# Kernel optimization log

Hardware: AMD Instinct MI355X
Metric: run time of the kernel (lower is better)

## Reference

```python
import jax, jax.numpy as jnp
import numpy as np

N = 50000   # nodes
E = 800000  # edges (avg degree 16)
IN, H, OUT = 128, 128, 128


def _lin(key, fan_in, fan_out):
    s = 1.0 / np.sqrt(fan_in)
    return jax.random.uniform(key, (fan_in, fan_out), minval=-s, maxval=s, dtype=jnp.float32)


def setup_inputs() -> dict:
    key = jax.random.key(0)
    ks = jax.random.split(key, 12)
    inp = {
        "x": jax.random.normal(ks[0], (N, IN), dtype=jnp.float32),
        "edge_index": jax.random.randint(ks[1], (2, E), 0, N, dtype=jnp.int64),
        # layer 1: in -> hidden
        "Wl1": _lin(ks[2], IN, H), "b1": jnp.zeros((H,), jnp.float32), "Wr1": _lin(ks[3], IN, H),
        # layer 2: hidden -> hidden
        "Wl2": _lin(ks[4], H, H), "b2": jnp.zeros((H,), jnp.float32), "Wr2": _lin(ks[5], H, H),
        # layer 3: hidden -> out
        "Wl3": _lin(ks[6], H, OUT), "b3": jnp.zeros((OUT,), jnp.float32), "Wr3": _lin(ks[7], H, OUT),
    }
    return inp


def _sage_conv(x, src, dst, inv_deg, Wl, b, Wr):
    # mean-aggregate neighbor messages: gather from src, scatter-sum to dst
    msg = jnp.take(x, src, axis=0)                       # [E, d]
    agg = jax.ops.segment_sum(msg, dst, num_segments=N)  # [N, d]
    mean = agg * inv_deg[:, None]                        # scatter-mean (0 for isolated)
    return mean @ Wl + b + x @ Wr


def reference(x, edge_index, Wl1, b1, Wr1, Wl2, b2, Wr2, Wl3, b3, Wr3):
    src, dst = edge_index[0], edge_index[1]
    deg = jax.ops.segment_sum(jnp.ones((E,), jnp.float32), dst, num_segments=N)
    inv_deg = jnp.where(deg > 0, 1.0 / jnp.maximum(deg, 1.0), 0.0)

    h = _sage_conv(x, src, dst, inv_deg, Wl1, b1, Wr1)
    h = jax.nn.relu(h)  # dropout p=0.5 is identity in eval mode
    h = _sage_conv(h, src, dst, inv_deg, Wl2, b2, Wr2)
    h = jax.nn.relu(h)
    h = _sage_conv(h, src, dst, inv_deg, Wl3, b3, Wr3)
    return h
```

## Files before the change

kernel.cpp:

```cpp
#include <hip/hip_runtime.h>


#define D 128

typedef __attribute__((ext_vector_type(8))) short bf16x8;
typedef __attribute__((ext_vector_type(4))) float f32x4;

__device__ inline ushort f2bf(float f) {
  union { float f; unsigned u; } v; v.f = f;
  unsigned r = v.u + 0x7fffu + ((v.u >> 16) & 1u);
  return (ushort)(r >> 16);
}
__device__ inline float bf2f(ushort h) {
  union { unsigned u; float f; } v; v.u = ((unsigned)h) << 16;
  return v.f;
}

__global__ __launch_bounds__(256) void k_bhist(const int* __restrict__ dst,
                                               int* __restrict__ bhist, int E, int NB) {
  __shared__ int h[512];
  int t = threadIdx.x;
  for (int i = t; i < NB; i += 256) h[i] = 0;
  __syncthreads();
  int beg = blockIdx.x * 4096;
  int end = min(beg + 4096, E);
  for (int i = beg + t; i < end; i += 256) atomicAdd(&h[dst[i] >> 7], 1);
  __syncthreads();
  for (int i = t; i < NB; i += 256)
    if (h[i]) atomicAdd(&bhist[i], h[i]);
}

__global__ __launch_bounds__(512) void k_bscan(const int* __restrict__ bhist,
                                               int* __restrict__ bbase,
                                               int* __restrict__ bcur,
                                               int* __restrict__ offN, int NB) {
  __shared__ int part[512];
  int t = threadIdx.x;
  part[t] = (t < NB) ? bhist[t] : 0;
  __syncthreads();
  for (int d = 1; d < 512; d <<= 1) {
    int x = part[t];
    int a = (t >= d) ? part[t - d] : 0;
    __syncthreads();
    part[t] = x + a;
    __syncthreads();
  }
  if (t < NB) {
    int b = (t == 0) ? 0 : part[t - 1];
    bbase[t] = b;
    bcur[t] = b;
  }
  if (t == NB - 1) *offN = part[t];
}

__global__ __launch_bounds__(256) void k_bucket(const int* __restrict__ src,
                                                const int* __restrict__ dst,
                                                int* __restrict__ bcur,
                                                unsigned* __restrict__ ebuf,
                                                int E, int NB) {
  __shared__ int h[512];
  __shared__ int base[512];
  int t = threadIdx.x;
  for (int i = t; i < NB; i += 256) h[i] = 0;
  __syncthreads();
  int beg = blockIdx.x * 4096;
  int end = min(beg + 4096, E);
  for (int i = beg + t; i < end; i += 256) atomicAdd(&h[dst[i] >> 7], 1);
  __syncthreads();
  for (int i = t; i < NB; i += 256) {
    int c = h[i];
    base[i] = c ? atomicAdd(&bcur[i], c) : 0;
    h[i] = 0;
  }
  __syncthreads();
  for (int i = beg + t; i < end; i += 256) {
    int d = dst[i];
    int b = d >> 7;
    int r = atomicAdd(&h[b], 1);
    ebuf[base[b] + r] = (((unsigned)src[i]) << 16) | (unsigned)d;
  }
}

__global__ __launch_bounds__(256) void k_csr(const unsigned* __restrict__ ebuf,
                                             const int* __restrict__ bbase,
                                             const int* __restrict__ bhist,
                                             int* __restrict__ off,
                                             float* __restrict__ invd,
                                             int* __restrict__ srcs, int N) {
  __shared__ int dcount[128];
  __shared__ int dloc[128];
  int b = blockIdx.x;
  int t = threadIdx.x;
  int beg = bbase[b];
  int end = beg + bhist[b];
  if (t < 128) dcount[t] = 0;
  __syncthreads();
  for (int i = beg + t; i < end; i += 256) atomicAdd(&dcount[ebuf[i] & 127], 1);
  __syncthreads();
  if (t < 128) dloc[t] = dcount[t];
  __syncthreads();
  for (int d = 1; d < 128; d <<= 1) {
    int x = 0, a = 0;
    if (t < 128) {
      x = dloc[t];
      if (t >= d) a = dloc[t - d];
    }
    __syncthreads();
    if (t < 128) dloc[t] = x + a;
    __syncthreads();
  }
  if (t < 128) {
    int node = b * 128 + t;
    if (node < N) {
      int ex = beg + dloc[t] - dcount[t];
      off[node] = ex;
      int c = dcount[t];
      invd[node] = c > 0 ? 1.0f / (float)c : 0.0f;
      dcount[t] = ex;
    }
  }
  __syncthreads();
  for (int i = beg + t; i < end; i += 256) {
    unsigned p = ebuf[i];
    int slot = atomicAdd(&dcount[p & 127], 1);
    srcs[slot] = (int)(p >> 16);
  }
}

__global__ void k_cast(const float* __restrict__ x, ushort* __restrict__ xb, int total4) {
  int i = blockIdx.x * blockDim.x + threadIdx.x;
  if (i >= total4) return;
  float4 v = *reinterpret_cast<const float4*>(x + (size_t)i * 4);
  ushort4 o;
  o.x = f2bf(v.x); o.y = f2bf(v.y); o.z = f2bf(v.z); o.w = f2bf(v.w);
  *reinterpret_cast<ushort4*>(xb + (size_t)i * 4) = o;
}

__global__ void k_pack3(const float* __restrict__ Wl1, const float* __restrict__ Wr1,
                        const float* __restrict__ Wl2, const float* __restrict__ Wr2,
                        const float* __restrict__ Wl3, const float* __restrict__ Wr3,
                        ushort* __restrict__ Bp) {
  int gidx = blockIdx.x * blockDim.x + threadIdx.x;
  int layer = gidx >> 15;
  int idx = gidx & 32767;
  const float* Wl = (layer == 0) ? Wl1 : (layer == 1) ? Wl2 : Wl3;
  const float* Wr = (layer == 0) ? Wr1 : (layer == 1) ? Wr2 : Wr3;
  int kk = idx >> 12;
  int ct = (idx >> 9) & 7;
  int l  = (idx >> 3) & 63;
  int j  = idx & 7;
  int k = kk * 32 + ((l >> 4) << 3) + j;
  int col = ct * 16 + (l & 15);
  float v = (k < 128) ? Wl[k * 128 + col] : Wr[(k - 128) * 128 + col];
  Bp[gidx] = f2bf(v);
}

__global__ __launch_bounds__(256) void k_gather(const ushort* __restrict__ hin,
                                                const int* __restrict__ off,
                                                const int* __restrict__ srcs,
                                                const float* __restrict__ invd,
                                                ushort* __restrict__ meanb, int N) {
  int wid = blockIdx.x * 4 + (threadIdx.x >> 6);
  if (wid >= N) return;
  int lane = threadIdx.x & 63;
  int g = lane >> 4;
  int s = lane & 15;
  int lo = off[wid], hi = off[wid + 1];

  float acc[8] = {0.f, 0.f, 0.f, 0.f, 0.f, 0.f, 0.f, 0.f};
  int e = lo + g;
  for (; e + 4 < hi; e += 8) {
    int i0 = srcs[e];
    int i1 = srcs[e + 4];
    bf16x8 v0 = *reinterpret_cast<const bf16x8*>(hin + (size_t)i0 * D + s * 8);
    bf16x8 v1 = *reinterpret_cast<const bf16x8*>(hin + (size_t)i1 * D + s * 8);
#pragma unroll
    for (int j = 0; j < 8; ++j) acc[j] += bf2f((ushort)v0[j]);
#pragma unroll
    for (int j = 0; j < 8; ++j) acc[j] += bf2f((ushort)v1[j]);
  }
  if (e < hi) {
    int i0 = srcs[e];
    bf16x8 v0 = *reinterpret_cast<const bf16x8*>(hin + (size_t)i0 * D + s * 8);
#pragma unroll
    for (int j = 0; j < 8; ++j) acc[j] += bf2f((ushort)v0[j]);
  }

#pragma unroll
  for (int j = 0; j < 8; ++j) acc[j] += __shfl_xor(acc[j], 16);
#pragma unroll
  for (int j = 0; j < 8; ++j) acc[j] += __shfl_xor(acc[j], 32);

  if (lane < 16) {
    float w = invd[wid];
    bf16x8 o;
#pragma unroll
    for (int j = 0; j < 8; ++j) o[j] = (short)f2bf(acc[j] * w);
    *reinterpret_cast<bf16x8*>(meanb + (size_t)wid * D + s * 8) = o;
  }
}

template <int RELU, int FINAL>
__global__ __launch_bounds__(256) void k_combine(const ushort* __restrict__ meanb,
                                                 const ushort* __restrict__ hb,
                                                 const ushort* __restrict__ Bpack,
                                                 const float* __restrict__ bias,
                                                 float* __restrict__ outf,
                                                 ushort* __restrict__ outh, int N) {
  int l = threadIdx.x & 63;
  int w = threadIdx.x >> 6;
  int row0 = blockIdx.x * 64 + w * 16;
  int lr = l & 15;
  int kgrp = l >> 4;
  int arow = row0 + lr;
  if (arow >= N) arow = N - 1;
  size_t abase = (size_t)arow * D;

  f32x4 acc[8];
#pragma unroll
  for (int ct = 0; ct < 8; ++ct) {
    float bv = bias[ct * 16 + lr];
    acc[ct] = (f32x4){bv, bv, bv, bv};
  }

#pragma unroll
  for (int kk = 0; kk < 8; ++kk) {
    const ushort* asrc = (kk < 4) ? meanb : hb;
    int klocal = ((kk & 3) << 5) + (kgrp << 3);
    bf16x8 a = *reinterpret_cast<const bf16x8*>(asrc + abase + klocal);
    const ushort* bb = Bpack + ((size_t)kk << 12) + ((size_t)l << 3);
#pragma unroll
    for (int ct = 0; ct < 8; ++ct) {
      bf16x8 b = *reinterpret_cast<const bf16x8*>(bb + (ct << 9));
      acc[ct] = __builtin_amdgcn_mfma_f32_16x16x32_bf16(a, b, acc[ct], 0, 0, 0);
    }
  }

#pragma unroll
  for (int ct = 0; ct < 8; ++ct) {
    int c = ct * 16 + lr;
#pragma unroll
    for (int r = 0; r < 4; ++r) {
      int rr = row0 + kgrp * 4 + r;
      if (rr < N) {
        float v = acc[ct][r];
        if (RELU) v = fmaxf(v, 0.f);
        if (FINAL) outf[(size_t)rr * D + c] = v;
        else outh[(size_t)rr * D + c] = f2bf(v);
      }
    }
  }
}

extern "C" void kernel_launch(void* const* d_in, const int* in_sizes, int n_in,
                              void* d_out, int out_size, void* d_ws, size_t ws_size,
                              hipStream_t stream) {
  const float* x   = (const float*)d_in[0];
  const int*   ei  = (const int*)d_in[1];
  const float* Wl1 = (const float*)d_in[2];
  const float* b1  = (const float*)d_in[3];
  const float* Wr1 = (const float*)d_in[4];
  const float* Wl2 = (const float*)d_in[5];
  const float* b2  = (const float*)d_in[6];
  const float* Wr2 = (const float*)d_in[7];
  const float* Wl3 = (const float*)d_in[8];
  const float* b3  = (const float*)d_in[9];
  const float* Wr3 = (const float*)d_in[10];
  float* out = (float*)d_out;

  int N = in_sizes[0] / D;
  int E = in_sizes[1] / 2;
  const int* srcp = ei;
  const int* dstp = ei + E;
  int NB = (N + 127) >> 7;

  char* p = (char*)d_ws;
  auto carve = [&](size_t bytes) {
    void* r = (void*)p;
    p += (bytes + 255) & ~(size_t)255;
    return r;
  };
  int*      bhist = (int*)carve((size_t)512 * 4);
  int*      bbase = (int*)carve((size_t)512 * 4);
  int*      bcur  = (int*)carve((size_t)512 * 4);
  int*      off   = (int*)carve((size_t)(N + 1) * 4);
  float*    invd  = (float*)carve((size_t)N * 4);
  int*      srcs  = (int*)carve((size_t)E * 4);
  unsigned* ebuf  = (unsigned*)carve((size_t)E * 4);
  ushort*   xb    = (ushort*)carve((size_t)N * D * 2);
  ushort*   h1b   = (ushort*)carve((size_t)N * D * 2);
  ushort*   h2b   = (ushort*)carve((size_t)N * D * 2);
  ushort*   meanb = (ushort*)carve((size_t)N * D * 2);
  ushort*   Bp    = (ushort*)carve((size_t)3 * 32768 * 2);

  hipMemsetAsync(bhist, 0, (size_t)NB * 4, stream);
  int ch_blocks = (E + 4095) / 4096;
  k_bhist<<<ch_blocks, 256, 0, stream>>>(dstp, bhist, E, NB);
  k_bscan<<<1, 512, 0, stream>>>(bhist, bbase, bcur, off + N, NB);
  k_bucket<<<ch_blocks, 256, 0, stream>>>(srcp, dstp, bcur, ebuf, E, NB);
  k_csr<<<NB, 256, 0, stream>>>(ebuf, bbase, bhist, off, invd, srcs, N);

  int total4 = N * D / 4;
  k_cast<<<(total4 + 255) / 256, 256, 0, stream>>>(x, xb, total4);
  k_pack3<<<3 * 32768 / 256, 256, 0, stream>>>(Wl1, Wr1, Wl2, Wr2, Wl3, Wr3, Bp);

  int gather_blocks  = (N + 3) / 4;
  int combine_blocks = (N + 63) / 64;

  k_gather<<<gather_blocks, 256, 0, stream>>>(xb, off, srcs, invd, meanb, N);
  k_combine<1, 0><<<combine_blocks, 256, 0, stream>>>(meanb, xb, Bp, b1, nullptr, h1b, N);
  k_gather<<<gather_blocks, 256, 0, stream>>>(h1b, off, srcs, invd, meanb, N);
  k_combine<1, 0><<<combine_blocks, 256, 0, stream>>>(meanb, h1b, Bp + 32768, b2, nullptr, h2b, N);
  k_gather<<<gather_blocks, 256, 0, stream>>>(h2b, off, srcs, invd, meanb, N);
  k_combine<0, 1><<<combine_blocks, 256, 0, stream>>>(meanb, h2b, Bp + 2 * 32768, b3, out, nullptr, N);
}
```

Measured before the change: 197.6 us.

## Fuse neighbor gather and MFMA combine into one kernel per layer

Merges the per-layer gather (mean aggregation) and combine (dual GEMM) kernels into one kernel. Each block aggregates 16 nodes into a swizzled LDS tile, then the four waves split the 128 output columns, two 16-wide tiles each. This removes the meanb round trip through global memory and half the launches. In exchange each block now does a small 16-row GEMM, so weight-fragment loads are amortized over fewer rows, and the gather and MFMA phases within a block are serialized by a barrier.

```diff
diff --git a/kernel.cpp b/kernel.cpp
--- a/kernel.cpp
+++ b/kernel.cpp
@@ -155,95 +155,102 @@
   Bp[gidx] = f2bf(v);
 }
 
-__global__ __launch_bounds__(256) void k_gather(const ushort* __restrict__ hin,
-                                                const int* __restrict__ off,
-                                                const int* __restrict__ srcs,
-                                                const float* __restrict__ invd,
-                                                ushort* __restrict__ meanb, int N) {
-  int wid = blockIdx.x * 4 + (threadIdx.x >> 6);
-  if (wid >= N) return;
-  int lane = threadIdx.x & 63;
+template <int RELU, int FINAL>
+__global__ __launch_bounds__(256, 6) void k_fused(const ushort* __restrict__ hin,
+                                                  const int* __restrict__ off,
+                                                  const int* __restrict__ srcs,
+                                                  const float* __restrict__ invd,
+                                                  const ushort* __restrict__ Bpack,
+                                                  const float* __restrict__ bias,
+                                                  float* __restrict__ outf,
+                                                  ushort* __restrict__ outh, int N) {
+  __shared__ ushort smean[16 * D];
+  int t = threadIdx.x;
+  int w = t >> 6;
+  int lane = t & 63;
+  int node0 = blockIdx.x * 16;
   int g = lane >> 4;
   int s = lane & 15;
-  int lo = off[wid], hi = off[wid + 1];
-
-  float acc[8] = {0.f, 0.f, 0.f, 0.f, 0.f, 0.f, 0.f, 0.f};
-  int e = lo + g;
-  for (; e + 4 < hi; e += 8) {
-    int i0 = srcs[e];
-    int i1 = srcs[e + 4];
-    bf16x8 v0 = *reinterpret_cast<const bf16x8*>(hin + (size_t)i0 * D + s * 8);
-    bf16x8 v1 = *reinterpret_cast<const bf16x8*>(hin + (size_t)i1 * D + s * 8);
-#pragma unroll
-    for (int j = 0; j < 8; ++j) acc[j] += bf2f((ushort)v0[j]);
-#pragma unroll
-    for (int j = 0; j < 8; ++j) acc[j] += bf2f((ushort)v1[j]);
-  }
-  if (e < hi) {
-    int i0 = srcs[e];
-    bf16x8 v0 = *reinterpret_cast<const bf16x8*>(hin + (size_t)i0 * D + s * 8);
-#pragma unroll
-    for (int j = 0; j < 8; ++j) acc[j] += bf2f((ushort)v0[j]);
-  }
-
-#pragma unroll
-  for (int j = 0; j < 8; ++j) acc[j] += __shfl_xor(acc[j], 16);
-#pragma unroll
-  for (int j = 0; j < 8; ++j) acc[j] += __shfl_xor(acc[j], 32);
-
-  if (lane < 16) {
-    float w = invd[wid];
-    bf16x8 o;
-#pragma unroll
-    for (int j = 0; j < 8; ++j) o[j] = (short)f2bf(acc[j] * w);
-    *reinterpret_cast<bf16x8*>(meanb + (size_t)wid * D + s * 8) = o;
-  }
-}
-
-template <int RELU, int FINAL>
-__global__ __launch_bounds__(256) void k_combine(const ushort* __restrict__ meanb,
-                                                 const ushort* __restrict__ hb,
-                                                 const ushort* __restrict__ Bpack,
-                                                 const float* __restrict__ bias,
-                                                 float* __restrict__ outf,
-                                                 ushort* __restrict__ outh, int N) {
-  int l = threadIdx.x & 63;
-  int w = threadIdx.x >> 6;
-  int row0 = blockIdx.x * 64 + w * 16;
-  int lr = l & 15;
-  int kgrp = l >> 4;
-  int arow = row0 + lr;
+
+  for (int q = 0; q < 4; ++q) {
+    int nl = w * 4 + q;
+    int n = node0 + nl;
+    float acc[8] = {0.f, 0.f, 0.f, 0.f, 0.f, 0.f, 0.f, 0.f};
+    float wgt = 0.f;
+    if (n < N) {
+      wgt = invd[n];
+      int lo = off[n], hi = off[n + 1];
+      int e = lo + g;
+      for (; e + 4 < hi; e += 8) {
+        int i0 = srcs[e];
+        int i1 = srcs[e + 4];
+        bf16x8 v0 = *reinterpret_cast<const bf16x8*>(hin + (size_t)i0 * D + s * 8);
+        bf16x8 v1 = *reinterpret_cast<const bf16x8*>(hin + (size_t)i1 * D + s * 8);
+#pragma unroll
+        for (int j = 0; j < 8; ++j) acc[j] += bf2f((ushort)v0[j]);
+#pragma unroll
+        for (int j = 0; j < 8; ++j) acc[j] += bf2f((ushort)v1[j]);
+      }
+      if (e < hi) {
+        int i0 = srcs[e];
+        bf16x8 v0 = *reinterpret_cast<const bf16x8*>(hin + (size_t)i0 * D + s * 8);
+#pragma unroll
+        for (int j = 0; j < 8; ++j) acc[j] += bf2f((ushort)v0[j]);
+      }
+    }
+#pragma unroll
+    for (int j = 0; j < 8; ++j) acc[j] += __shfl_xor(acc[j], 16);
+#pragma unroll
+    for (int j = 0; j < 8; ++j) acc[j] += __shfl_xor(acc[j], 32);
+    if (lane < 16) {
+      bf16x8 o;
+#pragma unroll
+      for (int j = 0; j < 8; ++j) o[j] = (short)f2bf(acc[j] * wgt);
+      int byte = nl * 256 + ((s * 16) ^ ((nl & 7) << 4));
+      *reinterpret_cast<bf16x8*>(reinterpret_cast<char*>(smean) + byte) = o;
+    }
+  }
+  __syncthreads();
+
+  int lr = lane & 15;
+  int kgrp = lane >> 4;
+  int arow = node0 + lr;
   if (arow >= N) arow = N - 1;
   size_t abase = (size_t)arow * D;
 
-  f32x4 acc[8];
-#pragma unroll
-  for (int ct = 0; ct < 8; ++ct) {
-    float bv = bias[ct * 16 + lr];
-    acc[ct] = (f32x4){bv, bv, bv, bv};
+  f32x4 acc2[2];
+#pragma unroll
+  for (int i = 0; i < 2; ++i) {
+    float bv = bias[(w * 2 + i) * 16 + lr];
+    acc2[i] = (f32x4){bv, bv, bv, bv};
   }
 
 #pragma unroll
   for (int kk = 0; kk < 8; ++kk) {
-    const ushort* asrc = (kk < 4) ? meanb : hb;
     int klocal = ((kk & 3) << 5) + (kgrp << 3);
-    bf16x8 a = *reinterpret_cast<const bf16x8*>(asrc + abase + klocal);
-    const ushort* bb = Bpack + ((size_t)kk << 12) + ((size_t)l << 3);
-#pragma unroll
-    for (int ct = 0; ct < 8; ++ct) {
-      bf16x8 b = *reinterpret_cast<const bf16x8*>(bb + (ct << 9));
-      acc[ct] = __builtin_amdgcn_mfma_f32_16x16x32_bf16(a, b, acc[ct], 0, 0, 0);
-    }
-  }
-
-#pragma unroll
-  for (int ct = 0; ct < 8; ++ct) {
-    int c = ct * 16 + lr;
+    bf16x8 a;
+    if (kk < 4) {
+      int byte = lr * 256 + ((klocal * 2) ^ ((lr & 7) << 4));
+      a = *reinterpret_cast<const bf16x8*>(reinterpret_cast<const char*>(smean) + byte);
+    } else {
+      a = *reinterpret_cast<const bf16x8*>(hin + abase + klocal);
+    }
+#pragma unroll
+    for (int i = 0; i < 2; ++i) {
+      int ct = w * 2 + i;
+      bf16x8 b = *reinterpret_cast<const bf16x8*>(Bpack + (((size_t)(kk * 8 + ct) * 64 + lane) << 3));
+      acc2[i] = __builtin_amdgcn_mfma_f32_16x16x32_bf16(a, b, acc2[i], 0, 0, 0);
+    }
+  }
+
+#pragma unroll
+  for (int i = 0; i < 2; ++i) {
+    int c = (w * 2 + i) * 16 + lr;
 #pragma unroll
     for (int r = 0; r < 4; ++r) {
-      int rr = row0 + kgrp * 4 + r;
+      int rr = node0 + kgrp * 4 + r;
       if (rr < N) {
-        float v = acc[ct][r];
+        float v = acc2[i][r];
         if (RELU) v = fmaxf(v, 0.f);
         if (FINAL) outf[(size_t)rr * D + c] = v;
         else outh[(size_t)rr * D + c] = f2bf(v);
@@ -290,7 +297,6 @@
   ushort*   xb    = (ushort*)carve((size_t)N * D * 2);
   ushort*   h1b   = (ushort*)carve((size_t)N * D * 2);
   ushort*   h2b   = (ushort*)carve((size_t)N * D * 2);
-  ushort*   meanb = (ushort*)carve((size_t)N * D * 2);
   ushort*   Bp    = (ushort*)carve((size_t)3 * 32768 * 2);
 
   hipMemsetAsync(bhist, 0, (size_t)NB * 4, stream);
@@ -304,13 +310,9 @@
   k_cast<<<(total4 + 255) / 256, 256, 0, stream>>>(x, xb, total4);
   k_pack3<<<3 * 32768 / 256, 256, 0, stream>>>(Wl1, Wr1, Wl2, Wr2, Wl3, Wr3, Bp);
 
-  int gather_blocks  = (N + 3) / 4;
-  int combine_blocks = (N + 63) / 64;
-
-  k_gather<<<gather_blocks, 256, 0, stream>>>(xb, off, srcs, invd, meanb, N);
-  k_combine<1, 0><<<combine_blocks, 256, 0, stream>>>(meanb, xb, Bp, b1, nullptr, h1b, N);
-  k_gather<<<gather_blocks, 256, 0, stream>>>(h1b, off, srcs, invd, meanb, N);
-  k_combine<1, 0><<<combine_blocks, 256, 0, stream>>>(meanb, h1b, Bp + 32768, b2, nullptr, h2b, N);
-  k_gather<<<gather_blocks, 256, 0, stream>>>(h2b, off, srcs, invd, meanb, N);
-  k_combine<0, 1><<<combine_blocks, 256, 0, stream>>>(meanb, h2b, Bp + 2 * 32768, b3, out, nullptr, N);
-}
+  int fused_blocks = (N + 15) / 16;
+
+  k_fused<1, 0><<<fused_blocks, 256, 0, stream>>>(xb, off, srcs, invd, Bp, b1, nullptr, h1b, N);
+  k_fused<1, 0><<<fused_blocks, 256, 0, stream>>>(h1b, off, srcs, invd, Bp + 32768, b2, nullptr, h2b, N);
+  k_fused<0, 1><<<fused_blocks, 256, 0, stream>>>(h2b, off, srcs, invd, Bp + 2 * 32768, b3, out, nullptr, N);
+}
```

After: 180.6 us. 1.09x faster.
